# Performance work log

Hardware: AMD Instinct MI355X
Metric: run time of the kernel (lower is better)

## Reference

```python
import jax, jax.numpy as jnp
import numpy as np
from jax import lax

VOL, PATCH, DIM, DEPTH, HEADS, DIM_HEAD, MLP, CH, B = 64, 8, 768, 4, 12, 64, 3072, 1, 2
INNER = HEADS * DIM_HEAD
GS = VOL // PATCH              # 8 -> N = 512 tokens
EPS = 1e-5


def _sincos_1d(embed_dim, pos):
    omega = np.arange(embed_dim // 2, dtype=float) / (embed_dim / 2.0)
    omega = 1.0 / 10000 ** omega
    out = np.einsum('m,d->md', pos.reshape(-1), omega)
    return np.concatenate([np.sin(out), np.cos(out)], axis=1)


def _pos_embed_3d(embed_dim, gs):
    gd = np.arange(gs, dtype=np.float32)
    gh = np.arange(gs, dtype=np.float32)
    gw = np.arange(gs, dtype=np.float32)
    grid = np.stack(np.meshgrid(gw, gh, gd), axis=0).reshape([3, 1, gs, gs, gs])
    emb = np.concatenate([_sincos_1d(embed_dim // 3, grid[i]) for i in range(3)], axis=1)
    return jnp.asarray(emb, jnp.float32)[None]  # [1, N, dim]


def setup_inputs() -> dict:
    key = jax.random.key(0)
    ks = jax.random.split(key, 12)
    s = 0.02  # xavier-like small init scale
    d = {
        'volume': jax.random.normal(ks[0], (B, CH, VOL, VOL, VOL), jnp.float32),
        'conv_w': jax.random.normal(ks[1], (DIM, CH, PATCH, PATCH, PATCH), jnp.float32) * s,
        'conv_b': jnp.zeros((DIM,), jnp.float32),
        'pos_embed': _pos_embed_3d(DIM, GS),
        'ln1_w': jnp.ones((DEPTH, DIM), jnp.float32),
        'ln1_b': jnp.zeros((DEPTH, DIM), jnp.float32),
        'w_qkv': jax.random.normal(ks[2], (DEPTH, DIM, 3 * INNER), jnp.float32) * s,
        'w_o': jax.random.normal(ks[3], (DEPTH, INNER, DIM), jnp.float32) * s,
        'b_o': jnp.zeros((DEPTH, DIM), jnp.float32),
        'ln2_w': jnp.ones((DEPTH, DIM), jnp.float32),
        'ln2_b': jnp.zeros((DEPTH, DIM), jnp.float32),
        'w1': jax.random.normal(ks[4], (DEPTH, DIM, MLP), jnp.float32) * s,
        'b1': jnp.zeros((DEPTH, MLP), jnp.float32),
        'w2': jax.random.normal(ks[5], (DEPTH, MLP, DIM), jnp.float32) * s,
        'b2': jnp.zeros((DEPTH, DIM), jnp.float32),
        'lnf_w': jnp.ones((DIM,), jnp.float32),
        'lnf_b': jnp.zeros((DIM,), jnp.float32),
    }
    return d


def _ln(x, w, b):
    m = jnp.mean(x, axis=-1, keepdims=True)
    v = jnp.mean(jnp.square(x - m), axis=-1, keepdims=True)
    return (x - m) * lax.rsqrt(v + EPS) * w + b


def _forward(volume, conv_w, conv_b, pos_embed, ln1_w, ln1_b, w_qkv, w_o, b_o,
             ln2_w, ln2_b, w1, b1, w2, b2, lnf_w, lnf_b):
    # Conv3d patch embedding (stride == kernel == patch)
    x = lax.conv_general_dilated(volume, conv_w, window_strides=(PATCH,) * 3,
                                 padding='VALID',
                                 dimension_numbers=('NCDHW', 'OIDHW', 'NCDHW'))
    x = x + conv_b[None, :, None, None, None]
    b = x.shape[0]
    x = x.reshape(b, DIM, -1).transpose(0, 2, 1)   # b (d h w) c -> [B, N, dim]
    x = x + pos_embed
    scale = DIM_HEAD ** -0.5

    def layer(x, p):
        l1w, l1b, wqkv, wo, bo, l2w, l2b, W1, B1, W2, B2 = p
        h = _ln(x, l1w, l1b)
        qkv = h @ wqkv                               # [B, N, 3*inner]
        q, k, v = jnp.split(qkv, 3, axis=-1)
        def heads(t):
            bsz, n, _ = t.shape
            return t.reshape(bsz, n, HEADS, DIM_HEAD).transpose(0, 2, 1, 3)
        q, k, v = heads(q), heads(k), heads(v)
        attn = jax.nn.softmax(jnp.einsum('bhqd,bhkd->bhqk', q, k) * scale, axis=-1)
        o = jnp.einsum('bhqk,bhkd->bhqd', attn, v)   # [B, H, N, dh]
        o = o.transpose(0, 2, 1, 3).reshape(x.shape[0], -1, INNER)
        x = x + (o @ wo + bo)
        h = _ln(x, l2w, l2b)
        x = x + (jnp.tanh(h @ W1 + B1) @ W2 + B2)
        return x, None

    params = (ln1_w, ln1_b, w_qkv, w_o, b_o, ln2_w, ln2_b, w1, b1, w2, b2)
    x, _ = lax.scan(layer, x, params)
    return _ln(x, lnf_w, lnf_b)


def reference(volume, conv_w, conv_b, pos_embed, ln1_w, ln1_b, w_qkv, w_o, b_o,
              ln2_w, ln2_b, w1, b1, w2, b2, lnf_w, lnf_b):
    return _forward(volume, conv_w, conv_b, pos_embed, ln1_w, ln1_b, w_qkv, w_o, b_o,
                    ln2_w, ln2_b, w1, b1, w2, b2, lnf_w, lnf_b)
```

## Files before the change

kernel.cpp:

```cpp
#include <hip/hip_runtime.h>
#include <hip/hip_bf16.h>

typedef __hip_bfloat16 bf16;
typedef short bf16x8 __attribute__((ext_vector_type(8)));
typedef float f32x4 __attribute__((ext_vector_type(4)));

__device__ __forceinline__ float b2f(bf16 v) { return __bfloat162float(v); }
__device__ __forceinline__ void storev(float* p, float v) { *p = v; }
__device__ __forceinline__ void storev(bf16* p, float v) { *p = __float2bfloat16(v); }

__device__ __forceinline__ void store4(float* p, float a, float b, float c, float d) {
  *(float4*)p = make_float4(a, b, c, d);
}
__device__ __forceinline__ void store4(bf16* p, float a, float b, float c, float d) {
  bf16 pk[4] = {__float2bfloat16(a), __float2bfloat16(b), __float2bfloat16(c),
                __float2bfloat16(d)};
  *(uint2*)p = *(uint2*)pk;
}

__device__ __forceinline__ void gl2lds16(const bf16* g, bf16* l) {
  __builtin_amdgcn_global_load_lds(
      (const __attribute__((address_space(1))) unsigned int*)g,
      (__attribute__((address_space(3))) unsigned int*)l, 16, 0, 0);
}
__device__ __forceinline__ void gl2lds16f(const float* g, float* l) {
  __builtin_amdgcn_global_load_lds(
      (const __attribute__((address_space(1))) unsigned int*)g,
      (__attribute__((address_space(3))) unsigned int*)l, 16, 0, 0);
}

__global__ void im2col_kernel(const float* __restrict__ vol, bf16* __restrict__ out) {
  int t = blockIdx.x;
  int b = t >> 9, n = t & 511;
  int pd = n >> 6, ph = (n >> 3) & 7, pw = n & 7;
  const float* vb = vol + ((size_t)b << 18);
  for (int l = threadIdx.x; l < 512; l += 256) {
    int i = l >> 6, j = (l >> 3) & 7, k = l & 7;
    out[(size_t)t * 512 + l] =
        __float2bfloat16(vb[(pd * 8 + i) * 4096 + (ph * 8 + j) * 64 + (pw * 8 + k)]);
  }
}

__global__ void convert_kernel(const float* __restrict__ in, bf16* __restrict__ out, int n) {
  int i = (blockIdx.x * 256 + threadIdx.x) * 4;
  if (i + 3 < n) {
    float4 v = *(const float4*)&in[i];
    out[i + 0] = __float2bfloat16(v.x);
    out[i + 1] = __float2bfloat16(v.y);
    out[i + 2] = __float2bfloat16(v.z);
    out[i + 3] = __float2bfloat16(v.w);
  }
}

__global__ __launch_bounds__(256) void transpose_all(
    const float* __restrict__ wqkv, const float* __restrict__ wo,
    const float* __restrict__ w1, const float* __restrict__ w2,
    bf16* __restrict__ tqkv, bf16* __restrict__ two,
    bf16* __restrict__ t1, bf16* __restrict__ t2) {
  int bid = blockIdx.x;
  size_t L = blockIdx.y;
  const float* in;
  bf16* out;
  int R, C, tc, t0;
  if (bid < 432)       { in = wqkv + L * 768 * 2304; out = tqkv + L * 768 * 2304; R = 768;  C = 2304; tc = 36; t0 = bid; }
  else if (bid < 576)  { in = wo + L * 768 * 768;    out = two + L * 768 * 768;   R = 768;  C = 768;  tc = 12; t0 = bid - 432; }
  else if (bid < 1152) { in = w1 + L * 768 * 3072;   out = t1 + L * 768 * 3072;   R = 768;  C = 3072; tc = 48; t0 = bid - 576; }
  else                 { in = w2 + L * 3072 * 768;   out = t2 + L * 3072 * 768;   R = 3072; C = 768;  tc = 12; t0 = bid - 1152; }
  int r0 = (t0 / tc) * 64, c0 = (t0 % tc) * 64;
  __shared__ float tile[4096];
  int tid = threadIdx.x;
#pragma unroll
  for (int it = 0; it < 4; ++it) {
    int s = tid + it * 256;
    int r = s >> 4, cc = s & 15;
    int csrc = (cc ^ ((r >> 3) & 7)) << 2;
    gl2lds16f(&in[(size_t)(r0 + r) * C + c0 + csrc], &tile[s * 4]);
  }
  __syncthreads();
  int cl = tid >> 3;
  int rb = (tid & 7) * 8;
  int xs = tid & 7;
#pragma unroll
  for (int half = 0; half < 2; ++half) {
    int c = cl + half * 32;
    int base = rb * 64 + (((c >> 2) ^ xs) << 2) + (c & 3);
    bf16 pk[8];
#pragma unroll
    for (int e = 0; e < 8; ++e) pk[e] = __float2bfloat16(tile[base + e * 64]);
    *(uint4*)&out[(size_t)(c0 + c) * R + r0 + rb] = *(uint4*)pk;
  }
}

template <typename OutT>
__global__ __launch_bounds__(256) void ln_kernel(const float* __restrict__ x,
                                                 const float* __restrict__ w,
                                                 const float* __restrict__ b,
                                                 OutT* __restrict__ out) {
  int row = (blockIdx.x << 2) + (threadIdx.x >> 6);
  int lane = threadIdx.x & 63;
  const float* xr = x + (size_t)row * 768;
  float4 v[3];
  float s = 0.f, ss = 0.f;
#pragma unroll
  for (int j = 0; j < 3; ++j) {
    v[j] = *(const float4*)&xr[j * 256 + lane * 4];
    s += v[j].x + v[j].y + v[j].z + v[j].w;
    ss += v[j].x * v[j].x + v[j].y * v[j].y + v[j].z * v[j].z + v[j].w * v[j].w;
  }
#pragma unroll
  for (int off = 32; off; off >>= 1) {
    s += __shfl_xor(s, off);
    ss += __shfl_xor(ss, off);
  }
  float m = s * (1.f / 768.f);
  float r = rsqrtf(ss * (1.f / 768.f) - m * m + 1e-5f);
  OutT* orow = out + (size_t)row * 768;
#pragma unroll
  for (int j = 0; j < 3; ++j) {
    int cidx = j * 256 + lane * 4;
    float4 wv = *(const float4*)&w[cidx];
    float4 bv = *(const float4*)&b[cidx];
    store4(orow + cidx,
           (v[j].x - m) * r * wv.x + bv.x,
           (v[j].y - m) * r * wv.y + bv.y,
           (v[j].z - m) * r * wv.z + bv.z,
           (v[j].w - m) * r * wv.w + bv.w);
  }
}

template <int BM, int BN, int EPI>
__global__ __launch_bounds__(256) void mfma_gemm(
    const bf16* __restrict__ A, const bf16* __restrict__ Bt,
    const float* __restrict__ bias, const float* __restrict__ aux,
    bf16* __restrict__ vt,
    void* __restrict__ Cout, int M, int N, int K) {
  constexpr int WTM = BM / 2, WTN = BN / 2;
  constexpr int MT = WTM / 16, NT = WTN / 16;
  __shared__ bf16 As[BM * 64];
  __shared__ bf16 Bs[BN * 64];
  int tid = threadIdx.x;
  int wave = tid >> 6, lane = tid & 63;
  int wm = wave >> 1, wn = wave & 1;
  int m15 = lane & 15, q = lane >> 4;
  int m0 = blockIdx.y * BM, n0 = blockIdx.x * BN;
  int kspan = K / gridDim.z;
  int kbeg = blockIdx.z * kspan, kend = kbeg + kspan;

  f32x4 acc[MT][NT];
#pragma unroll
  for (int i = 0; i < MT; ++i)
#pragma unroll
    for (int j = 0; j < NT; ++j) acc[i][j] = (f32x4){0.f, 0.f, 0.f, 0.f};

  for (int k0 = kbeg; k0 < kend; k0 += 64) {
#pragma unroll
    for (int it = 0; it < BM * 8 / 256; ++it) {
      int c = tid + it * 256;
      int row = c >> 3, cc = c & 7;
      gl2lds16(&A[(size_t)(m0 + row) * K + k0 + cc * 8], &As[c * 8]);
    }
#pragma unroll
    for (int it = 0; it < BN * 8 / 256; ++it) {
      int c = tid + it * 256;
      int row = c >> 3, cc = c & 7;
      gl2lds16(&Bt[(size_t)(n0 + row) * K + k0 + cc * 8], &Bs[c * 8]);
    }
    __syncthreads();
#pragma unroll
    for (int s = 0; s < 2; ++s) {
      bf16x8 af[MT], bfr[NT];
#pragma unroll
      for (int i = 0; i < MT; ++i)
        af[i] = *(const bf16x8*)&As[(wm * WTM + i * 16 + m15) * 64 + s * 32 + q * 8];
#pragma unroll
      for (int j = 0; j < NT; ++j)
        bfr[j] = *(const bf16x8*)&Bs[(wn * WTN + j * 16 + m15) * 64 + s * 32 + q * 8];
#pragma unroll
      for (int i = 0; i < MT; ++i)
#pragma unroll
        for (int j = 0; j < NT; ++j)
          acc[i][j] = __builtin_amdgcn_mfma_f32_16x16x32_bf16(af[i], bfr[j], acc[i][j], 0, 0, 0);
    }
    __syncthreads();
  }

#pragma unroll
  for (int i = 0; i < MT; ++i) {
#pragma unroll
    for (int j = 0; j < NT; ++j) {
      int col = n0 + wn * WTN + j * 16 + m15;
      if (EPI == 4) {
        if (col < 1536) {
#pragma unroll
          for (int r = 0; r < 4; ++r) {
            int row = m0 + wm * WTM + i * 16 + q * 4 + r;
            ((bf16*)Cout)[(size_t)row * 1536 + col] = __float2bfloat16(acc[i][j][r]);
          }
        } else {
          int row0 = m0 + wm * WTM + i * 16 + q * 4;
          int cl = col - 1536;
          int hh = cl >> 6, dd = cl & 63;
          int bb = row0 >> 9, tok = row0 & 511;
          bf16 pk[4];
#pragma unroll
          for (int r = 0; r < 4; ++r) pk[r] = __float2bfloat16(acc[i][j][r]);
          *(uint2*)&vt[((size_t)(bb * 12 + hh) * 64 + dd) * 512 + tok] = *(uint2*)pk;
        }
      } else if (EPI == 5) {
        float bv = (blockIdx.z == 0) ? bias[col] : 0.f;
#pragma unroll
        for (int r = 0; r < 4; ++r) {
          int row = m0 + wm * WTM + i * 16 + q * 4 + r;
          unsafeAtomicAdd(&((float*)Cout)[(size_t)row * N + col], acc[i][j][r] + bv);
        }
      } else {
        float bv = (EPI == 0) ? 0.f : bias[col];
#pragma unroll
        for (int r = 0; r < 4; ++r) {
          int row = m0 + wm * WTM + i * 16 + q * 4 + r;
          float v = acc[i][j][r] + bv;
          if (EPI == 2) v = tanhf(v);
          if (EPI == 3) v += aux[(size_t)(row & 511) * N + col];
          if (EPI == 0 || EPI == 2)
            ((bf16*)Cout)[(size_t)row * N + col] = __float2bfloat16(v);
          else
            ((float*)Cout)[(size_t)row * N + col] = v;
        }
      }
    }
  }
}

__global__ __launch_bounds__(128) void attn_mfma(const bf16* __restrict__ qk,
                                                 const bf16* __restrict__ Vt,
                                                 bf16* __restrict__ o) {
  constexpr int PS = 520;
  __shared__ bf16 KVs[64 * 64];
  __shared__ bf16 P[32 * PS];
  int bh = blockIdx.x;
  int b = bh / 12, hh = bh % 12;
  int q0 = blockIdx.y * 32;
  int tid = threadIdx.x;
  int wave = tid >> 6, lane = tid & 63;
  int n15 = lane & 15, quad = lane >> 4;
  const bf16* qkb = qk + (size_t)b * 512 * 1536;
  int ql = wave * 16 + n15;

  const bf16* qp = qkb + (size_t)(q0 + ql) * 1536 + hh * 64 + quad * 8;
  bf16x8 qf0 = *(const bf16x8*)qp;
  bf16x8 qf1 = *(const bf16x8*)(qp + 32);

  f32x4 S[32];
#pragma unroll
  for (int i = 0; i < 32; ++i) S[i] = (f32x4){0.f, 0.f, 0.f, 0.f};

  const bf16* kbase = qkb + 768 + hh * 64;
#pragma unroll
  for (int kc = 0; kc < 8; ++kc) {
    __syncthreads();
#pragma unroll
    for (int it = 0; it < 4; ++it) {
      int c = tid + it * 128;
      int r = c >> 3, cc = c & 7;
      gl2lds16(&kbase[(size_t)(kc * 64 + r) * 1536 + cc * 8], &KVs[c * 8]);
    }
    __syncthreads();
#pragma unroll
    for (int t = 0; t < 4; ++t) {
      int idx = kc * 4 + t;
      bf16x8 a0 = *(const bf16x8*)&KVs[(t * 16 + n15) * 64 + quad * 8];
      bf16x8 a1 = *(const bf16x8*)&KVs[(t * 16 + n15) * 64 + 32 + quad * 8];
      S[idx] = __builtin_amdgcn_mfma_f32_16x16x32_bf16(a0, qf0, S[idx], 0, 0, 0);
      S[idx] = __builtin_amdgcn_mfma_f32_16x16x32_bf16(a1, qf1, S[idx], 0, 0, 0);
    }
  }

  float mx = -1e30f;
#pragma unroll
  for (int i = 0; i < 32; ++i)
#pragma unroll
    for (int r = 0; r < 4; ++r) { S[i][r] *= 0.125f; mx = fmaxf(mx, S[i][r]); }
  mx = fmaxf(mx, __shfl_xor(mx, 16));
  mx = fmaxf(mx, __shfl_xor(mx, 32));
  float sum = 0.f;
#pragma unroll
  for (int i = 0; i < 32; ++i)
#pragma unroll
    for (int r = 0; r < 4; ++r) { float e = __expf(S[i][r] - mx); S[i][r] = e; sum += e; }
  sum += __shfl_xor(sum, 16);
  sum += __shfl_xor(sum, 32);
  float inv = 1.f / sum;

#pragma unroll
  for (int i = 0; i < 32; ++i) {
    bf16 pk[4];
#pragma unroll
    for (int r = 0; r < 4; ++r) pk[r] = __float2bfloat16(S[i][r] * inv);
    *(uint2*)&P[(size_t)ql * PS + i * 16 + quad * 4] = *(uint2*)pk;
  }

  f32x4 oacc[4];
#pragma unroll
  for (int dt = 0; dt < 4; ++dt) oacc[dt] = (f32x4){0.f, 0.f, 0.f, 0.f};
  const bf16* vtb = Vt + (size_t)bh * 64 * 512;
  for (int kc = 0; kc < 8; ++kc) {
    __syncthreads();
#pragma unroll
    for (int it = 0; it < 4; ++it) {
      int c = tid + it * 128;
      int r = c >> 3, cc = c & 7;
      gl2lds16(&vtb[(size_t)r * 512 + kc * 64 + cc * 8], &KVs[c * 8]);
    }
    __syncthreads();
    bf16x8 p0 = *(const bf16x8*)&P[(size_t)ql * PS + kc * 64 + quad * 8];
    bf16x8 p1 = *(const bf16x8*)&P[(size_t)ql * PS + kc * 64 + 32 + quad * 8];
#pragma unroll
    for (int dt = 0; dt < 4; ++dt) {
      bf16x8 v0 = *(const bf16x8*)&KVs[(dt * 16 + n15) * 64 + quad * 8];
      bf16x8 v1 = *(const bf16x8*)&KVs[(dt * 16 + n15) * 64 + 32 + quad * 8];
      oacc[dt] = __builtin_amdgcn_mfma_f32_16x16x32_bf16(p0, v0, oacc[dt], 0, 0, 0);
      oacc[dt] = __builtin_amdgcn_mfma_f32_16x16x32_bf16(p1, v1, oacc[dt], 0, 0, 0);
    }
  }

#pragma unroll
  for (int dt = 0; dt < 4; ++dt)
#pragma unroll
    for (int r = 0; r < 4; ++r) {
      int tok = q0 + wave * 16 + quad * 4 + r;
      o[((size_t)b * 512 + tok) * 768 + hh * 64 + dt * 16 + n15] =
          __float2bfloat16(oacc[dt][r]);
    }
}

extern "C" void kernel_launch(void* const* d_in, const int* in_sizes, int n_in,
                              void* d_out, int out_size, void* d_ws, size_t ws_size,
                              hipStream_t stream) {
  const float* volume = (const float*)d_in[0];
  const float* conv_w = (const float*)d_in[1];
  const float* conv_b = (const float*)d_in[2];
  const float* pos    = (const float*)d_in[3];
  const float* ln1w   = (const float*)d_in[4];
  const float* ln1b   = (const float*)d_in[5];
  const float* wqkv   = (const float*)d_in[6];
  const float* wo     = (const float*)d_in[7];
  const float* bo     = (const float*)d_in[8];
  const float* ln2w   = (const float*)d_in[9];
  const float* ln2b   = (const float*)d_in[10];
  const float* w1     = (const float*)d_in[11];
  const float* b1     = (const float*)d_in[12];
  const float* w2     = (const float*)d_in[13];
  const float* b2     = (const float*)d_in[14];
  const float* lnfw   = (const float*)d_in[15];
  const float* lnfb   = (const float*)d_in[16];

  char* w = (char*)d_ws;
  float* x    = (float*)(w + 0);
  bf16* h     = (bf16*)(w + 3145728);
  bf16* qk    = (bf16*)(w + 4718592);
  bf16* patchA= qk;
  bf16* Vt    = (bf16*)(w + 7864320);
  bf16* oact  = (bf16*)(w + 9437184);
  bf16* cwb   = (bf16*)(w + 15728640);
  bf16* tqkv  = (bf16*)(w + 16515072);
  bf16* two   = (bf16*)(w + 30670848);
  bf16* t1    = (bf16*)(w + 35389440);
  bf16* t2    = (bf16*)(w + 54263808);

  convert_kernel<<<384, 256, 0, stream>>>(conv_w, cwb, 768 * 512);
  im2col_kernel<<<1024, 256, 0, stream>>>(volume, patchA);
  transpose_all<<<dim3(1728, 4), 256, 0, stream>>>(wqkv, wo, w1, w2, tqkv, two, t1, t2);
  mfma_gemm<64, 64, 3><<<dim3(12, 16), 256, 0, stream>>>(
      patchA, cwb, conv_b, pos, nullptr, x, 1024, 768, 512);

  for (int L = 0; L < 4; ++L) {
    ln_kernel<bf16><<<256, 256, 0, stream>>>(x, ln1w + L * 768, ln1b + L * 768, h);
    mfma_gemm<64, 64, 4><<<dim3(36, 16), 256, 0, stream>>>(
        h, tqkv + (size_t)L * 768 * 2304, nullptr, nullptr, Vt, qk, 1024, 2304, 768);
    attn_mfma<<<dim3(24, 16), 128, 0, stream>>>(qk, Vt, oact);
    mfma_gemm<64, 64, 5><<<dim3(12, 16, 2), 256, 0, stream>>>(
        oact, two + (size_t)L * 768 * 768, bo + L * 768, nullptr, nullptr, x, 1024, 768, 768);
    ln_kernel<bf16><<<256, 256, 0, stream>>>(x, ln2w + L * 768, ln2b + L * 768, h);
    mfma_gemm<64, 64, 2><<<dim3(48, 16), 256, 0, stream>>>(
        h, t1 + (size_t)L * 768 * 3072, b1 + L * 3072, nullptr, nullptr, oact, 1024, 3072, 768);
    mfma_gemm<64, 64, 5><<<dim3(12, 16, 4), 256, 0, stream>>>(
        oact, t2 + (size_t)L * 768 * 3072, b2 + L * 768, nullptr, nullptr, x, 1024, 768, 3072);
  }

  ln_kernel<float><<<256, 256, 0, stream>>>(x, lnfw, lnfb, (float*)d_out);
}
```

Before: 506.0 us.

## Double-buffer weight transpose across four tiles and use taller GEMM tiles

New measurement: 548.7 us. 8.4% more time.

```diff
diff --git a/kernel.cpp b/kernel.cpp
--- a/kernel.cpp
+++ b/kernel.cpp
@@ -52,42 +52,74 @@
   }
 }
 
+struct TP { const float* in; bf16* out; int R, C, r0, c0; };
+
+__device__ __forceinline__ TP tp_params(int bid, size_t L,
+    const float* wqkv, const float* wo, const float* w1, const float* w2,
+    bf16* tqkv, bf16* two, bf16* t1, bf16* t2) {
+  TP p;
+  int tc, t0;
+  if (bid < 432)       { p.in = wqkv + L * 768 * 2304; p.out = tqkv + L * 768 * 2304; p.R = 768;  p.C = 2304; tc = 36; t0 = bid; }
+  else if (bid < 576)  { p.in = wo + L * 768 * 768;    p.out = two + L * 768 * 768;   p.R = 768;  p.C = 768;  tc = 12; t0 = bid - 432; }
+  else if (bid < 1152) { p.in = w1 + L * 768 * 3072;   p.out = t1 + L * 768 * 3072;   p.R = 768;  p.C = 3072; tc = 48; t0 = bid - 576; }
+  else                 { p.in = w2 + L * 3072 * 768;   p.out = t2 + L * 3072 * 768;   p.R = 3072; p.C = 768;  tc = 12; t0 = bid - 1152; }
+  p.r0 = (t0 / tc) * 64;
+  p.c0 = (t0 % tc) * 64;
+  return p;
+}
+
+__device__ __forceinline__ void tp_stage(const TP& p, float* buf, int tid) {
+#pragma unroll
+  for (int it = 0; it < 4; ++it) {
+    int s = tid + it * 256;
+    int r = s >> 4, cc = s & 15;
+    int csrc = (cc ^ ((r >> 3) & 7)) << 2;
+    gl2lds16f(&p.in[(size_t)(p.r0 + r) * p.C + p.c0 + csrc], &buf[s * 4]);
+  }
+}
+
+__device__ __forceinline__ void tp_process(const TP& p, const float* buf, int tid) {
+  int cl = tid >> 3, rb = (tid & 7) * 8, xs = tid & 7;
+#pragma unroll
+  for (int half = 0; half < 2; ++half) {
+    int c = cl + half * 32;
+    int base = rb * 64 + (((c >> 2) ^ xs) << 2) + (c & 3);
+    bf16 pk[8];
+#pragma unroll
+    for (int e = 0; e < 8; ++e) pk[e] = __float2bfloat16(buf[base + e * 64]);
+    *(uint4*)&p.out[(size_t)(p.c0 + c) * p.R + p.r0 + rb] = *(uint4*)pk;
+  }
+}
+
 __global__ __launch_bounds__(256) void transpose_all(
     const float* __restrict__ wqkv, const float* __restrict__ wo,
     const float* __restrict__ w1, const float* __restrict__ w2,
     bf16* __restrict__ tqkv, bf16* __restrict__ two,
     bf16* __restrict__ t1, bf16* __restrict__ t2) {
-  int bid = blockIdx.x;
+  __shared__ float tile[2][4096];
+  int tid = threadIdx.x;
   size_t L = blockIdx.y;
-  const float* in;
-  bf16* out;
-  int R, C, tc, t0;
-  if (bid < 432)       { in = wqkv + L * 768 * 2304; out = tqkv + L * 768 * 2304; R = 768;  C = 2304; tc = 36; t0 = bid; }
-  else if (bid < 576)  { in = wo + L * 768 * 768;    out = two + L * 768 * 768;   R = 768;  C = 768;  tc = 12; t0 = bid - 432; }
-  else if (bid < 1152) { in = w1 + L * 768 * 3072;   out = t1 + L * 768 * 3072;   R = 768;  C = 3072; tc = 48; t0 = bid - 576; }
-  else                 { in = w2 + L * 3072 * 768;   out = t2 + L * 3072 * 768;   R = 3072; C = 768;  tc = 12; t0 = bid - 1152; }
-  int r0 = (t0 / tc) * 64, c0 = (t0 % tc) * 64;
-  __shared__ float tile[4096];
-  int tid = threadIdx.x;
-#pragma unroll
-  for (int it = 0; it < 4; ++it) {
-    int s = tid + it * 256;
-    int r = s >> 4, cc = s & 15;
-    int csrc = (cc ^ ((r >> 3) & 7)) << 2;
-    gl2lds16f(&in[(size_t)(r0 + r) * C + c0 + csrc], &tile[s * 4]);
-  }
-  __syncthreads();
-  int cl = tid >> 3;
-  int rb = (tid & 7) * 8;
-  int xs = tid & 7;
-#pragma unroll
-  for (int half = 0; half < 2; ++half) {
-    int c = cl + half * 32;
-    int base = rb * 64 + (((c >> 2) ^ xs) << 2) + (c & 3);
-    bf16 pk[8];
-#pragma unroll
-    for (int e = 0; e < 8; ++e) pk[e] = __float2bfloat16(tile[base + e * 64]);
-    *(uint4*)&out[(size_t)(c0 + c) * R + r0 + rb] = *(uint4*)pk;
+  int b0 = blockIdx.x * 4;
+
+  TP p0 = tp_params(b0, L, wqkv, wo, w1, w2, tqkv, two, t1, t2);
+  tp_stage(p0, tile[0], tid);
+  asm volatile("s_waitcnt vmcnt(0)" ::: "memory");
+  __builtin_amdgcn_s_barrier();
+  __builtin_amdgcn_sched_barrier(0);
+
+#pragma unroll
+  for (int t = 0; t < 4; ++t) {
+    if (t < 3) {
+      TP pn = tp_params(b0 + t + 1, L, wqkv, wo, w1, w2, tqkv, two, t1, t2);
+      tp_stage(pn, tile[(t + 1) & 1], tid);
+    }
+    TP pc = tp_params(b0 + t, L, wqkv, wo, w1, w2, tqkv, two, t1, t2);
+    tp_process(pc, tile[t & 1], tid);
+    if (t < 3) {
+      asm volatile("s_waitcnt vmcnt(2)" ::: "memory");
+      __builtin_amdgcn_s_barrier();
+      __builtin_amdgcn_sched_barrier(0);
+    }
   }
 }
 
@@ -128,19 +160,19 @@
   }
 }
 
-template <int BM, int BN, int EPI>
+template <int BM, int BN, int WR, int WC, int EPI>
 __global__ __launch_bounds__(256) void mfma_gemm(
     const bf16* __restrict__ A, const bf16* __restrict__ Bt,
     const float* __restrict__ bias, const float* __restrict__ aux,
     bf16* __restrict__ vt,
     void* __restrict__ Cout, int M, int N, int K) {
-  constexpr int WTM = BM / 2, WTN = BN / 2;
+  constexpr int WTM = BM / WR, WTN = BN / WC;
   constexpr int MT = WTM / 16, NT = WTN / 16;
   __shared__ bf16 As[BM * 64];
   __shared__ bf16 Bs[BN * 64];
   int tid = threadIdx.x;
   int wave = tid >> 6, lane = tid & 63;
-  int wm = wave >> 1, wn = wave & 1;
+  int wm = wave / WC, wn = wave % WC;
   int m15 = lane & 15, q = lane >> 4;
   int m0 = blockIdx.y * BM, n0 = blockIdx.x * BN;
   int kspan = K / gridDim.z;
@@ -369,21 +401,21 @@
 
   convert_kernel<<<384, 256, 0, stream>>>(conv_w, cwb, 768 * 512);
   im2col_kernel<<<1024, 256, 0, stream>>>(volume, patchA);
-  transpose_all<<<dim3(1728, 4), 256, 0, stream>>>(wqkv, wo, w1, w2, tqkv, two, t1, t2);
-  mfma_gemm<64, 64, 3><<<dim3(12, 16), 256, 0, stream>>>(
+  transpose_all<<<dim3(432, 4), 256, 0, stream>>>(wqkv, wo, w1, w2, tqkv, two, t1, t2);
+  mfma_gemm<64, 64, 2, 2, 3><<<dim3(12, 16), 256, 0, stream>>>(
       patchA, cwb, conv_b, pos, nullptr, x, 1024, 768, 512);
 
   for (int L = 0; L < 4; ++L) {
     ln_kernel<bf16><<<256, 256, 0, stream>>>(x, ln1w + L * 768, ln1b + L * 768, h);
-    mfma_gemm<64, 64, 4><<<dim3(36, 16), 256, 0, stream>>>(
+    mfma_gemm<128, 64, 4, 1, 4><<<dim3(36, 8), 256, 0, stream>>>(
         h, tqkv + (size_t)L * 768 * 2304, nullptr, nullptr, Vt, qk, 1024, 2304, 768);
     attn_mfma<<<dim3(24, 16), 128, 0, stream>>>(qk, Vt, oact);
-    mfma_gemm<64, 64, 5><<<dim3(12, 16, 2), 256, 0, stream>>>(
+    mfma_gemm<64, 64, 2, 2, 5><<<dim3(12, 16, 2), 256, 0, stream>>>(
         oact, two + (size_t)L * 768 * 768, bo + L * 768, nullptr, nullptr, x, 1024, 768, 768);
     ln_kernel<bf16><<<256, 256, 0, stream>>>(x, ln2w + L * 768, ln2b + L * 768, h);
-    mfma_gemm<64, 64, 2><<<dim3(48, 16), 256, 0, stream>>>(
+    mfma_gemm<128, 64, 4, 1, 2><<<dim3(48, 8), 256, 0, stream>>>(
         h, t1 + (size_t)L * 768 * 3072, b1 + L * 3072, nullptr, nullptr, oact, 1024, 3072, 768);
-    mfma_gemm<64, 64, 5><<<dim3(12, 16, 4), 256, 0, stream>>>(
+    mfma_gemm<128, 64, 4, 1, 5><<<dim3(12, 8, 4), 256, 0, stream>>>(
         oact, t2 + (size_t)L * 768 * 3072, b2 + L * 768, nullptr, nullptr, x, 1024, 768, 3072);
   }
 
```
